# Optimization experiments

Hardware: AMD Instinct MI355X
Metric: run time of the kernel (lower is better)

Reference implementation:

```python
import jax, jax.numpy as jnp
import numpy as np

N = 100000       # nodes
E = 1600000      # edges (avg degree 16)
IN_DIM = 128
HIDDEN = 128


def _glorot(key, shape):
    s = 1.0 / np.sqrt(shape[0])
    return jax.random.uniform(key, shape, minval=-s, maxval=s, dtype=jnp.float32)


def setup_inputs() -> dict:
    key = jax.random.key(0)
    ks = jax.random.split(key, 8)
    x = jax.random.normal(ks[0], (N, IN_DIM), dtype=jnp.float32)
    edge_index = jax.random.randint(ks[1], (2, E), 0, N, dtype=jnp.int32)
    W0 = _glorot(ks[2], (IN_DIM, HIDDEN))
    b0 = jnp.zeros((HIDDEN,), dtype=jnp.float32)
    W1 = _glorot(ks[3], (HIDDEN, HIDDEN))
    b1 = jnp.zeros((HIDDEN,), dtype=jnp.float32)
    W2 = _glorot(ks[4], (HIDDEN, HIDDEN))
    b2 = jnp.zeros((HIDDEN,), dtype=jnp.float32)
    return {"x": x, "edge_index": edge_index,
            "W0": W0, "b0": b0, "W1": W1, "b1": b1, "W2": W2, "b2": b2}


def _gcn_conv(x, row, col, norm, W, b):
    # x' = W x, then out[i] = sum_{j in N(i) U {i}} norm_ji * x'[j], + bias
    h = x @ W                              # [N, out]
    msg = norm[:, None] * h[row]           # [E+N, out] gather + scale
    out = jax.ops.segment_sum(msg, col, num_segments=N)  # scatter-add
    return out + b


def reference(x, edge_index, W0, b0, W1, b1, W2, b2):
    # PyG GCNConv default: add self-loops, symmetric normalization D^-1/2 A D^-1/2
    self_loops = jnp.arange(N, dtype=edge_index.dtype)
    row = jnp.concatenate([edge_index[0], self_loops])  # sources
    col = jnp.concatenate([edge_index[1], self_loops])  # destinations
    deg = jax.ops.segment_sum(jnp.ones_like(col, dtype=x.dtype), col, num_segments=N)
    dinv = jax.lax.rsqrt(deg)              # deg >= 1 thanks to self-loops
    norm = dinv[row] * dinv[col]           # [E+N]

    h = _gcn_conv(x, row, col, norm, W0, b0)
    h = jax.nn.relu(h)                     # dropout: eval mode (identity)
    h = _gcn_conv(h, row, col, norm, W1, b1)
    h = jax.nn.relu(h)
    return _gcn_conv(h, row, col, norm, W2, b2)
```

## Files before the change

### kernel.cpp

```cpp
#include <hip/hip_runtime.h>

#define HID 128
#define BR  128
#define FILL_CHUNK 2048

typedef _Float16 f16;
typedef f16 f16x2 __attribute__((ext_vector_type(2)));
typedef f16 f16x4 __attribute__((ext_vector_type(4)));
typedef f16 f16x8 __attribute__((ext_vector_type(8)));
typedef float f32x4 __attribute__((ext_vector_type(4)));

static __device__ __forceinline__ float2 h2f(unsigned int u) {
    f16x2 v;
    __builtin_memcpy(&v, &u, 4);
    return make_float2((float)v[0], (float)v[1]);
}


__global__ void k_deg_count(const int* __restrict__ col, int* __restrict__ cnt, int E, int N) {
    const int xcd = blockIdx.x & 7;
    const int chunk = blockIdx.x >> 3;
    const int per = (N + 7) >> 3;
    const int lo = xcd * per;
    const int hi = min(N, lo + per);
    const int eend = min(E, (chunk + 1) * FILL_CHUNK);
    for (int e = chunk * FILL_CHUNK + threadIdx.x; e < eend; e += 256) {
        int c = col[e];
        if (c >= lo && c < hi) atomicAdd(&cnt[c], 1);
    }
}

__global__ void k_scan_block(const int* __restrict__ cnt, int* __restrict__ excl,
                             int* __restrict__ bsum, float* __restrict__ dinv, int N) {
    __shared__ int s[256];
    int i = blockIdx.x * 256 + threadIdx.x;
    int v = (i < N) ? cnt[i] : 0;
    if (i < N) dinv[i] = 1.0f / sqrtf((float)(v + 1));
    s[threadIdx.x] = v;
    __syncthreads();
    for (int off = 1; off < 256; off <<= 1) {
        int t = (threadIdx.x >= off) ? s[threadIdx.x - off] : 0;
        __syncthreads();
        s[threadIdx.x] += t;
        __syncthreads();
    }
    if (i < N) excl[i] = s[threadIdx.x] - v;
    if (threadIdx.x == 255) bsum[blockIdx.x] = s[255];
}

__global__ __launch_bounds__(1024) void k_scan_bsum(int* __restrict__ bsum, int nb) {
    __shared__ int s[1024];
    int i = threadIdx.x;
    int v = (i < nb) ? bsum[i] : 0;
    s[i] = v;
    __syncthreads();
    for (int off = 1; off < 1024; off <<= 1) {
        int t = (i >= off) ? s[i - off] : 0;
        __syncthreads();
        s[i] += t;
        __syncthreads();
    }
    if (i < nb) bsum[i] = s[i] - v;
}

__global__ void k_scan_add(int* __restrict__ row_ptr, const int* __restrict__ bsum,
                           int* __restrict__ fill, int N, int E) {
    int i = blockIdx.x * 256 + threadIdx.x;
    if (i < N) {
        int v = row_ptr[i] + bsum[blockIdx.x];
        row_ptr[i] = v;
        fill[i] = v;
    }
    if (i == 0) row_ptr[N] = E;
}

__global__ void k_fill(const int* __restrict__ row, const int* __restrict__ col,
                       int* __restrict__ fill, int* __restrict__ csr_src, int E, int N) {
    const int xcd = blockIdx.x & 7;
    const int chunk = blockIdx.x >> 3;
    const int per = (N + 7) >> 3;
    const int lo = xcd * per;
    const int hi = min(N, lo + per);
    const int eend = min(E, (chunk + 1) * FILL_CHUNK);
    for (int e = chunk * FILL_CHUNK + threadIdx.x; e < eend; e += 256) {
        int c = col[e];
        if (c >= lo && c < hi) {
            int p = atomicAdd(&fill[c], 1);
            csr_src[p] = row[e];
        }
    }
}


__global__ void k_wprep3(const float* __restrict__ W0, const float* __restrict__ W1,
                         const float* __restrict__ W2, f16* __restrict__ out) {
    const int b = blockIdx.x;
    const int which = b >> 4;
    const float* W = which == 0 ? W0 : (which == 1 ? W1 : W2);
    f16* o = out + which * 32768;
    int i = (b & 15) * 256 + threadIdx.x;
    int k = i >> 5, n0 = (i & 31) * 4;
    float4 v = reinterpret_cast<const float4*>(W)[i];
    float vv[4] = {v.x, v.y, v.z, v.w};
#pragma unroll
    for (int e = 0; e < 4; ++e) {
        int n = n0 + e;
        int idx = (k >> 3) * 1024 + n * 8 + (k & 7);
        f16 h = (f16)vv[e];
        o[idx] = h;
        o[16384 + idx] = (f16)(vv[e] - (float)h);
    }
}


template<int MODE>
__global__ __launch_bounds__(512, 4) void k_gemm(const void* __restrict__ Xv,
                                                 const f16* __restrict__ Wt,
                                                 const float* __restrict__ dinv,
                                                 f16* __restrict__ H, int N) {
    __shared__ f16 Xs[MODE == 0 ? 2 * 16384 : 16384];
    const int t = threadIdx.x;
    const int row0 = blockIdx.x * BR;

    const int w  = t >> 6;
    const int l  = t & 63;
    const int lg = l >> 4;
    const int li = l & 15;
    const int ng = w & 3;
    const int mg = w >> 2;

    f16x8 Wh[2][4], Wl[2][4];
#pragma unroll
    for (int nb = 0; nb < 2; ++nb) {
        const int ncol = (ng * 2 + nb) * 16 + li;
#pragma unroll
        for (int ks = 0; ks < 4; ++ks) {
            const int idx = (ks * 4 + lg) * 1024 + ncol * 8;
            Wh[nb][ks] = *reinterpret_cast<const f16x8*>(&Wt[idx]);
            Wl[nb][ks] = *reinterpret_cast<const f16x8*>(&Wt[16384 + idx]);
        }
    }

    if constexpr (MODE == 0) {
        const float* X = (const float*)Xv;
        for (int i = t; i < 4096; i += 512) {
            int r = i >> 5, q = i & 31;
            int gr = row0 + r;
            float4 v = make_float4(0.f, 0.f, 0.f, 0.f);
            if (gr < N) v = reinterpret_cast<const float4*>(X + (size_t)gr * HID)[q];
            f16 h0 = (f16)v.x, h1 = (f16)v.y, h2 = (f16)v.z, h3 = (f16)v.w;
            f16 l0 = (f16)(v.x - (float)h0), l1 = (f16)(v.y - (float)h1);
            f16 l2 = (f16)(v.z - (float)h2), l3 = (f16)(v.w - (float)h3);
            int base = r * 128 + (((q >> 1) ^ (r & 7)) * 8) + (q & 1) * 4;
            *reinterpret_cast<f16x4*>(&Xs[base])         = (f16x4){h0, h1, h2, h3};
            *reinterpret_cast<f16x4*>(&Xs[16384 + base]) = (f16x4){l0, l1, l2, l3};
        }
    } else {
        const f16* src = (const f16*)Xv + (size_t)row0 * HID;
        for (int i = t; i < 2048; i += 512)
            *reinterpret_cast<f16x8*>(&Xs[i * 8]) = *reinterpret_cast<const f16x8*>(src + (size_t)i * 8);
    }
    __syncthreads();

    f32x4 acc[2][4];
#pragma unroll
    for (int nb = 0; nb < 2; ++nb)
#pragma unroll
        for (int mb = 0; mb < 4; ++mb) acc[nb][mb] = (f32x4){0.f, 0.f, 0.f, 0.f};

#pragma unroll
    for (int mb = 0; mb < 4; ++mb) {
        const int arow = mg * 64 + mb * 16 + li;
#pragma unroll
        for (int ks = 0; ks < 4; ++ks) {
            const int idx = arow * 128 + (((ks * 4 + lg) ^ (arow & 7)) * 8);
            f16x8 Xh = *reinterpret_cast<const f16x8*>(&Xs[idx]);
#pragma unroll
            for (int nb = 0; nb < 2; ++nb) {
                acc[nb][mb] = __builtin_amdgcn_mfma_f32_16x16x32_f16(Wh[nb][ks], Xh, acc[nb][mb], 0, 0, 0);
                acc[nb][mb] = __builtin_amdgcn_mfma_f32_16x16x32_f16(Wl[nb][ks], Xh, acc[nb][mb], 0, 0, 0);
            }
            if constexpr (MODE == 0) {
                f16x8 Xl = *reinterpret_cast<const f16x8*>(&Xs[16384 + idx]);
#pragma unroll
                for (int nb = 0; nb < 2; ++nb)
                    acc[nb][mb] = __builtin_amdgcn_mfma_f32_16x16x32_f16(Wh[nb][ks], Xl, acc[nb][mb], 0, 0, 0);
            }
        }
    }

#pragma unroll
    for (int mb = 0; mb < 4; ++mb) {
        const int m = row0 + mg * 64 + mb * 16 + li;
        if (m < N) {
            const float d = dinv[m];
#pragma unroll
            for (int nb = 0; nb < 2; ++nb) {
                f16x4 o = {(f16)(acc[nb][mb][0] * d), (f16)(acc[nb][mb][1] * d),
                           (f16)(acc[nb][mb][2] * d), (f16)(acc[nb][mb][3] * d)};
                *reinterpret_cast<f16x4*>(&H[(size_t)m * HID + (ng * 2 + nb) * 16 + lg * 4]) = o;
            }
        }
    }
}


template<bool F16OUT>
__global__ __launch_bounds__(256) void k_agg_csr(const f16* __restrict__ h,
                                                 const int* __restrict__ csr_src,
                                                 const int* __restrict__ row_ptr,
                                                 const float* __restrict__ dinv,
                                                 const float* __restrict__ bias,
                                                 void* __restrict__ outv, int N) {
    const int node = blockIdx.x * 8 + (threadIdx.x >> 5);
    if (node >= N) return;
    const int l = threadIdx.x & 31;
    const uint2* h2 = reinterpret_cast<const uint2*>(h);

    uint2 us = h2[(size_t)node * 32 + l];
    float2 a0 = h2f(us.x), a1 = h2f(us.y);
    float acc0 = a0.x, acc1 = a0.y, acc2 = a1.x, acc3 = a1.y;

    int j = row_ptr[node];
    const int end = row_ptr[node + 1];

    for (; j + 8 <= end; j += 8) {
        int s0 = csr_src[j];
        int s1 = csr_src[j + 1];
        int s2 = csr_src[j + 2];
        int s3 = csr_src[j + 3];
        int s4 = csr_src[j + 4];
        int s5 = csr_src[j + 5];
        int s6 = csr_src[j + 6];
        int s7 = csr_src[j + 7];
        uint2 u0 = h2[(size_t)s0 * 32 + l];
        uint2 u1 = h2[(size_t)s1 * 32 + l];
        uint2 u2 = h2[(size_t)s2 * 32 + l];
        uint2 u3 = h2[(size_t)s3 * 32 + l];
        uint2 u4 = h2[(size_t)s4 * 32 + l];
        uint2 u5 = h2[(size_t)s5 * 32 + l];
        uint2 u6 = h2[(size_t)s6 * 32 + l];
        uint2 u7 = h2[(size_t)s7 * 32 + l];
        float2 v0 = h2f(u0.x), w0 = h2f(u0.y), v1 = h2f(u1.x), w1 = h2f(u1.y);
        float2 v2 = h2f(u2.x), w2 = h2f(u2.y), v3 = h2f(u3.x), w3 = h2f(u3.y);
        float2 v4 = h2f(u4.x), w4 = h2f(u4.y), v5 = h2f(u5.x), w5 = h2f(u5.y);
        float2 v6 = h2f(u6.x), w6 = h2f(u6.y), v7 = h2f(u7.x), w7 = h2f(u7.y);
        acc0 += ((v0.x + v1.x) + (v2.x + v3.x)) + ((v4.x + v5.x) + (v6.x + v7.x));
        acc1 += ((v0.y + v1.y) + (v2.y + v3.y)) + ((v4.y + v5.y) + (v6.y + v7.y));
        acc2 += ((w0.x + w1.x) + (w2.x + w3.x)) + ((w4.x + w5.x) + (w6.x + w7.x));
        acc3 += ((w0.y + w1.y) + (w2.y + w3.y)) + ((w4.y + w5.y) + (w6.y + w7.y));
    }
    for (; j < end; ++j) {
        uint2 u = h2[(size_t)csr_src[j] * 32 + l];
        float2 v = h2f(u.x), w = h2f(u.y);
        acc0 += v.x; acc1 += v.y; acc2 += w.x; acc3 += w.y;
    }

    const float di = dinv[node];
    const float4 bv = reinterpret_cast<const float4*>(bias)[l];
    float o0 = fmaf(di, acc0, bv.x);
    float o1 = fmaf(di, acc1, bv.y);
    float o2 = fmaf(di, acc2, bv.z);
    float o3 = fmaf(di, acc3, bv.w);

    if constexpr (F16OUT) {
        o0 = fmaxf(o0, 0.f); o1 = fmaxf(o1, 0.f);
        o2 = fmaxf(o2, 0.f); o3 = fmaxf(o3, 0.f);
        const int swz = (((l >> 1) ^ (node & 7)) << 1) | (l & 1);
        f16x4 o = {(f16)o0, (f16)o1, (f16)o2, (f16)o3};
        *reinterpret_cast<f16x4*>((f16*)outv + (size_t)node * HID + swz * 4) = o;
    } else {
        *reinterpret_cast<float4*>((float*)outv + (size_t)node * HID + l * 4) =
            make_float4(o0, o1, o2, o3);
    }
}


extern "C" void kernel_launch(void* const* d_in, const int* in_sizes, int n_in,
                              void* d_out, int out_size, void* d_ws, size_t ws_size,
                              hipStream_t stream) {
    const float* x  = (const float*)d_in[0];
    const int*   ei = (const int*)  d_in[1];
    const float* W0 = (const float*)d_in[2];
    const float* b0 = (const float*)d_in[3];
    const float* W1 = (const float*)d_in[4];
    const float* b1 = (const float*)d_in[5];
    const float* W2 = (const float*)d_in[6];
    const float* b2 = (const float*)d_in[7];

    const int N = in_sizes[0] / HID;
    const int E = in_sizes[1] / 2;
    const int* row = ei;
    const int* col = ei + E;

    const int nb_n = (N + 255) / 256;

    f16*   h16     = (f16*)d_ws;
    float* dinv    = (float*)(h16 + (size_t)N * HID);
    int*   cnt     = (int*)(dinv + N);
    int*   row_ptr = cnt + N;
    int*   fill    = row_ptr + (N + 1);
    int*   bsum    = fill + N;
    int*   csr_src = bsum + nb_n;
    f16*   wt      = (f16*)(csr_src + E);
    f16*   wt0     = wt;
    f16*   wt1     = wt + 32768;
    f16*   wt2     = wt + 65536;
    f16*   act     = (f16*)d_out;
    float* out     = (float*)d_out;

    const int nb_gemm = (N + BR - 1) / BR;
    const int nb_agg  = (N + 7) / 8;
    const int nb_fill = ((E + FILL_CHUNK - 1) / FILL_CHUNK) * 8;

    hipMemsetAsync(cnt, 0, (size_t)N * sizeof(int), stream);
    k_wprep3<<<48, 256, 0, stream>>>(W0, W1, W2, wt);
    k_deg_count <<<nb_fill, 256, 0, stream>>>(col, cnt, E, N);
    k_scan_block<<<nb_n, 256, 0, stream>>>(cnt, row_ptr, bsum, dinv, N);
    k_scan_bsum <<<1, 1024, 0, stream>>>(bsum, nb_n);
    k_scan_add  <<<nb_n, 256, 0, stream>>>(row_ptr, bsum, fill, N, E);
    k_fill      <<<nb_fill, 256, 0, stream>>>(row, col, fill, csr_src, E, N);

    k_gemm<0>      <<<nb_gemm, 512, 0, stream>>>(x, wt0, dinv, h16, N);
    k_agg_csr<true><<<nb_agg, 256, 0, stream>>>(h16, csr_src, row_ptr, dinv, b0, act, N);
    k_gemm<1>      <<<nb_gemm, 512, 0, stream>>>(act, wt1, dinv, h16, N);
    k_agg_csr<true><<<nb_agg, 256, 0, stream>>>(h16, csr_src, row_ptr, dinv, b1, act, N);
    k_gemm<1>      <<<nb_gemm, 512, 0, stream>>>(act, wt2, dinv, h16, N);
    k_agg_csr<false><<<nb_agg, 256, 0, stream>>>(h16, csr_src, row_ptr, dinv, b2, out, N);
}
```

Before: 424.2 us.

## Widen aggregation to 16 lanes per node, privatize degree counts per XCD

The CSR aggregation kernel now uses 16 threads per node, each loading 16-byte uint4 (eight f16 features), with eight accumulators and a matching 8-wide swizzled or float store. This halves the threads per node and widens each gather load. Degree counting drops the 8x per-XCD filtering pass and instead atomically adds into eight private count arrays, which the scan then sums. Index streams use nontemporal loads. In exchange it needs 8N extra ints of workspace and a larger memset, and the swizzle pattern of the f16 output changes, which must match what the GEMM reader expects.

New measurement: 446.4 us. +5.2%, slower.

```diff
diff --git a/kernel.cpp b/kernel.cpp
--- a/kernel.cpp
+++ b/kernel.cpp
@@ -17,25 +17,23 @@
 }
 
 
-__global__ void k_deg_count(const int* __restrict__ col, int* __restrict__ cnt, int E, int N) {
-    const int xcd = blockIdx.x & 7;
-    const int chunk = blockIdx.x >> 3;
-    const int per = (N + 7) >> 3;
-    const int lo = xcd * per;
-    const int hi = min(N, lo + per);
-    const int eend = min(E, (chunk + 1) * FILL_CHUNK);
-    for (int e = chunk * FILL_CHUNK + threadIdx.x; e < eend; e += 256) {
-        int c = col[e];
-        if (c >= lo && c < hi) atomicAdd(&cnt[c], 1);
-    }
-}
-
-__global__ void k_scan_block(const int* __restrict__ cnt, int* __restrict__ excl,
+__global__ void k_deg_count(const int* __restrict__ col, int* __restrict__ cnt8, int E, int N) {
+    int* cnt = cnt8 + (size_t)(blockIdx.x & 7) * N;
+    const int eend = min(E, (blockIdx.x + 1) * FILL_CHUNK);
+    for (int e = blockIdx.x * FILL_CHUNK + threadIdx.x; e < eend; e += 256)
+        atomicAdd(&cnt[__builtin_nontemporal_load(col + e)], 1);
+}
+
+__global__ void k_scan_block(const int* __restrict__ cnt8, int* __restrict__ excl,
                              int* __restrict__ bsum, float* __restrict__ dinv, int N) {
     __shared__ int s[256];
     int i = blockIdx.x * 256 + threadIdx.x;
-    int v = (i < N) ? cnt[i] : 0;
-    if (i < N) dinv[i] = 1.0f / sqrtf((float)(v + 1));
+    int v = 0;
+    if (i < N) {
+#pragma unroll
+        for (int x = 0; x < 8; ++x) v += cnt8[(size_t)x * N + i];
+        dinv[i] = 1.0f / sqrtf((float)(v + 1));
+    }
     s[threadIdx.x] = v;
     __syncthreads();
     for (int off = 1; off < 256; off <<= 1) {
@@ -83,10 +81,10 @@
     const int hi = min(N, lo + per);
     const int eend = min(E, (chunk + 1) * FILL_CHUNK);
     for (int e = chunk * FILL_CHUNK + threadIdx.x; e < eend; e += 256) {
-        int c = col[e];
+        int c = __builtin_nontemporal_load(col + e);
         if (c >= lo && c < hi) {
             int p = atomicAdd(&fill[c], 1);
-            csr_src[p] = row[e];
+            csr_src[p] = __builtin_nontemporal_load(row + e);
         }
     }
 }
@@ -212,66 +210,81 @@
                                                  const float* __restrict__ dinv,
                                                  const float* __restrict__ bias,
                                                  void* __restrict__ outv, int N) {
-    const int node = blockIdx.x * 8 + (threadIdx.x >> 5);
+    const int node = blockIdx.x * 16 + (threadIdx.x >> 4);
     if (node >= N) return;
-    const int l = threadIdx.x & 31;
-    const uint2* h2 = reinterpret_cast<const uint2*>(h);
-
-    uint2 us = h2[(size_t)node * 32 + l];
-    float2 a0 = h2f(us.x), a1 = h2f(us.y);
+    const int l = threadIdx.x & 15;
+    const uint4* h4 = reinterpret_cast<const uint4*>(h);
+
+    uint4 us = h4[(size_t)node * 16 + l];
+    float2 a0 = h2f(us.x), a1 = h2f(us.y), a2 = h2f(us.z), a3 = h2f(us.w);
     float acc0 = a0.x, acc1 = a0.y, acc2 = a1.x, acc3 = a1.y;
+    float acc4 = a2.x, acc5 = a2.y, acc6 = a3.x, acc7 = a3.y;
 
     int j = row_ptr[node];
     const int end = row_ptr[node + 1];
 
     for (; j + 8 <= end; j += 8) {
-        int s0 = csr_src[j];
-        int s1 = csr_src[j + 1];
-        int s2 = csr_src[j + 2];
-        int s3 = csr_src[j + 3];
-        int s4 = csr_src[j + 4];
-        int s5 = csr_src[j + 5];
-        int s6 = csr_src[j + 6];
-        int s7 = csr_src[j + 7];
-        uint2 u0 = h2[(size_t)s0 * 32 + l];
-        uint2 u1 = h2[(size_t)s1 * 32 + l];
-        uint2 u2 = h2[(size_t)s2 * 32 + l];
-        uint2 u3 = h2[(size_t)s3 * 32 + l];
-        uint2 u4 = h2[(size_t)s4 * 32 + l];
-        uint2 u5 = h2[(size_t)s5 * 32 + l];
-        uint2 u6 = h2[(size_t)s6 * 32 + l];
-        uint2 u7 = h2[(size_t)s7 * 32 + l];
-        float2 v0 = h2f(u0.x), w0 = h2f(u0.y), v1 = h2f(u1.x), w1 = h2f(u1.y);
-        float2 v2 = h2f(u2.x), w2 = h2f(u2.y), v3 = h2f(u3.x), w3 = h2f(u3.y);
-        float2 v4 = h2f(u4.x), w4 = h2f(u4.y), v5 = h2f(u5.x), w5 = h2f(u5.y);
-        float2 v6 = h2f(u6.x), w6 = h2f(u6.y), v7 = h2f(u7.x), w7 = h2f(u7.y);
-        acc0 += ((v0.x + v1.x) + (v2.x + v3.x)) + ((v4.x + v5.x) + (v6.x + v7.x));
-        acc1 += ((v0.y + v1.y) + (v2.y + v3.y)) + ((v4.y + v5.y) + (v6.y + v7.y));
-        acc2 += ((w0.x + w1.x) + (w2.x + w3.x)) + ((w4.x + w5.x) + (w6.x + w7.x));
-        acc3 += ((w0.y + w1.y) + (w2.y + w3.y)) + ((w4.y + w5.y) + (w6.y + w7.y));
+        int s0 = __builtin_nontemporal_load(csr_src + j);
+        int s1 = __builtin_nontemporal_load(csr_src + j + 1);
+        int s2 = __builtin_nontemporal_load(csr_src + j + 2);
+        int s3 = __builtin_nontemporal_load(csr_src + j + 3);
+        int s4 = __builtin_nontemporal_load(csr_src + j + 4);
+        int s5 = __builtin_nontemporal_load(csr_src + j + 5);
+        int s6 = __builtin_nontemporal_load(csr_src + j + 6);
+        int s7 = __builtin_nontemporal_load(csr_src + j + 7);
+        uint4 u0 = h4[(size_t)s0 * 16 + l];
+        uint4 u1 = h4[(size_t)s1 * 16 + l];
+        uint4 u2 = h4[(size_t)s2 * 16 + l];
+        uint4 u3 = h4[(size_t)s3 * 16 + l];
+        uint4 u4 = h4[(size_t)s4 * 16 + l];
+        uint4 u5 = h4[(size_t)s5 * 16 + l];
+        uint4 u6 = h4[(size_t)s6 * 16 + l];
+        uint4 u7 = h4[(size_t)s7 * 16 + l];
+#pragma unroll
+        for (int q = 0; q < 1; ++q) { }
+        float2 t;
+        t = h2f(u0.x); acc0 += t.x; acc1 += t.y;  t = h2f(u0.y); acc2 += t.x; acc3 += t.y;
+        t = h2f(u0.z); acc4 += t.x; acc5 += t.y;  t = h2f(u0.w); acc6 += t.x; acc7 += t.y;
+        t = h2f(u1.x); acc0 += t.x; acc1 += t.y;  t = h2f(u1.y); acc2 += t.x; acc3 += t.y;
+        t = h2f(u1.z); acc4 += t.x; acc5 += t.y;  t = h2f(u1.w); acc6 += t.x; acc7 += t.y;
+        t = h2f(u2.x); acc0 += t.x; acc1 += t.y;  t = h2f(u2.y); acc2 += t.x; acc3 += t.y;
+        t = h2f(u2.z); acc4 += t.x; acc5 += t.y;  t = h2f(u2.w); acc6 += t.x; acc7 += t.y;
+        t = h2f(u3.x); acc0 += t.x; acc1 += t.y;  t = h2f(u3.y); acc2 += t.x; acc3 += t.y;
+        t = h2f(u3.z); acc4 += t.x; acc5 += t.y;  t = h2f(u3.w); acc6 += t.x; acc7 += t.y;
+        t = h2f(u4.x); acc0 += t.x; acc1 += t.y;  t = h2f(u4.y); acc2 += t.x; acc3 += t.y;
+        t = h2f(u4.z); acc4 += t.x; acc5 += t.y;  t = h2f(u4.w); acc6 += t.x; acc7 += t.y;
+        t = h2f(u5.x); acc0 += t.x; acc1 += t.y;  t = h2f(u5.y); acc2 += t.x; acc3 += t.y;
+        t = h2f(u5.z); acc4 += t.x; acc5 += t.y;  t = h2f(u5.w); acc6 += t.x; acc7 += t.y;
+        t = h2f(u6.x); acc0 += t.x; acc1 += t.y;  t = h2f(u6.y); acc2 += t.x; acc3 += t.y;
+        t = h2f(u6.z); acc4 += t.x; acc5 += t.y;  t = h2f(u6.w); acc6 += t.x; acc7 += t.y;
+        t = h2f(u7.x); acc0 += t.x; acc1 += t.y;  t = h2f(u7.y); acc2 += t.x; acc3 += t.y;
+        t = h2f(u7.z); acc4 += t.x; acc5 += t.y;  t = h2f(u7.w); acc6 += t.x; acc7 += t.y;
     }
     for (; j < end; ++j) {
-        uint2 u = h2[(size_t)csr_src[j] * 32 + l];
-        float2 v = h2f(u.x), w = h2f(u.y);
-        acc0 += v.x; acc1 += v.y; acc2 += w.x; acc3 += w.y;
+        int s = __builtin_nontemporal_load(csr_src + j);
+        uint4 u = h4[(size_t)s * 16 + l];
+        float2 t;
+        t = h2f(u.x); acc0 += t.x; acc1 += t.y;  t = h2f(u.y); acc2 += t.x; acc3 += t.y;
+        t = h2f(u.z); acc4 += t.x; acc5 += t.y;  t = h2f(u.w); acc6 += t.x; acc7 += t.y;
     }
 
     const float di = dinv[node];
-    const float4 bv = reinterpret_cast<const float4*>(bias)[l];
-    float o0 = fmaf(di, acc0, bv.x);
-    float o1 = fmaf(di, acc1, bv.y);
-    float o2 = fmaf(di, acc2, bv.z);
-    float o3 = fmaf(di, acc3, bv.w);
+    const float4 bv0 = reinterpret_cast<const float4*>(bias)[l * 2];
+    const float4 bv1 = reinterpret_cast<const float4*>(bias)[l * 2 + 1];
+    float o0 = fmaf(di, acc0, bv0.x), o1 = fmaf(di, acc1, bv0.y);
+    float o2 = fmaf(di, acc2, bv0.z), o3 = fmaf(di, acc3, bv0.w);
+    float o4 = fmaf(di, acc4, bv1.x), o5 = fmaf(di, acc5, bv1.y);
+    float o6 = fmaf(di, acc6, bv1.z), o7 = fmaf(di, acc7, bv1.w);
 
     if constexpr (F16OUT) {
-        o0 = fmaxf(o0, 0.f); o1 = fmaxf(o1, 0.f);
-        o2 = fmaxf(o2, 0.f); o3 = fmaxf(o3, 0.f);
-        const int swz = (((l >> 1) ^ (node & 7)) << 1) | (l & 1);
-        f16x4 o = {(f16)o0, (f16)o1, (f16)o2, (f16)o3};
-        *reinterpret_cast<f16x4*>((f16*)outv + (size_t)node * HID + swz * 4) = o;
+        f16x8 o = {(f16)fmaxf(o0, 0.f), (f16)fmaxf(o1, 0.f), (f16)fmaxf(o2, 0.f),
+                   (f16)fmaxf(o3, 0.f), (f16)fmaxf(o4, 0.f), (f16)fmaxf(o5, 0.f),
+                   (f16)fmaxf(o6, 0.f), (f16)fmaxf(o7, 0.f)};
+        *reinterpret_cast<f16x8*>((f16*)outv + (size_t)node * HID + (l ^ (node & 7)) * 8) = o;
     } else {
-        *reinterpret_cast<float4*>((float*)outv + (size_t)node * HID + l * 4) =
-            make_float4(o0, o1, o2, o3);
+        float* op = (float*)outv + (size_t)node * HID + l * 8;
+        *reinterpret_cast<float4*>(op)     = make_float4(o0, o1, o2, o3);
+        *reinterpret_cast<float4*>(op + 4) = make_float4(o4, o5, o6, o7);
     }
 }
 
@@ -297,8 +310,8 @@
 
     f16*   h16     = (f16*)d_ws;
     float* dinv    = (float*)(h16 + (size_t)N * HID);
-    int*   cnt     = (int*)(dinv + N);
-    int*   row_ptr = cnt + N;
+    int*   cnt8    = (int*)(dinv + N);
+    int*   row_ptr = cnt8 + (size_t)8 * N;
     int*   fill    = row_ptr + (N + 1);
     int*   bsum    = fill + N;
     int*   csr_src = bsum + nb_n;
@@ -309,14 +322,15 @@
     f16*   act     = (f16*)d_out;
     float* out     = (float*)d_out;
 
-    const int nb_gemm = (N + BR - 1) / BR;
-    const int nb_agg  = (N + 7) / 8;
-    const int nb_fill = ((E + FILL_CHUNK - 1) / FILL_CHUNK) * 8;
-
-    hipMemsetAsync(cnt, 0, (size_t)N * sizeof(int), stream);
+    const int nb_gemm  = (N + BR - 1) / BR;
+    const int nb_agg   = (N + 15) / 16;
+    const int nb_chunk = (E + FILL_CHUNK - 1) / FILL_CHUNK;
+    const int nb_fill  = nb_chunk * 8;
+
+    hipMemsetAsync(cnt8, 0, (size_t)8 * N * sizeof(int), stream);
     k_wprep3<<<48, 256, 0, stream>>>(W0, W1, W2, wt);
-    k_deg_count <<<nb_fill, 256, 0, stream>>>(col, cnt, E, N);
-    k_scan_block<<<nb_n, 256, 0, stream>>>(cnt, row_ptr, bsum, dinv, N);
+    k_deg_count <<<nb_chunk, 256, 0, stream>>>(col, cnt8, E, N);
+    k_scan_block<<<nb_n, 256, 0, stream>>>(cnt8, row_ptr, bsum, dinv, N);
     k_scan_bsum <<<1, 1024, 0, stream>>>(bsum, nb_n);
     k_scan_add  <<<nb_n, 256, 0, stream>>>(row_ptr, bsum, fill, N, E);
     k_fill      <<<nb_fill, 256, 0, stream>>>(row, col, fill, csr_src, E, N);
```
